# Kernel optimization log

Measured on AMD Instinct MI355X. Metric: run time of the kernel, lower is better.

The kernel has to match this reference:

```python
import jax, jax.numpy as jnp
import numpy as np
import math

H = 16
D_MODEL = 1024
D_K = 64
BS = 8
SEQ = 1024


def setup_inputs() -> dict:
    key = jax.random.key(0)
    ks = jax.random.split(key, 13)
    s = 1.0 / math.sqrt(D_MODEL)
    inp = {
        "q": jax.random.normal(ks[0], (BS, SEQ, D_MODEL), dtype=jnp.float32),
        "k": jax.random.normal(ks[1], (BS, SEQ, D_MODEL), dtype=jnp.float32),
        "v": jax.random.normal(ks[2], (BS, SEQ, D_MODEL), dtype=jnp.float32),
        "mask": jax.random.randint(ks[3], (BS, SEQ, SEQ), 0, 2, dtype=jnp.int32),
        "Wq": jax.random.normal(ks[4], (D_MODEL, D_MODEL), dtype=jnp.float32) * s,
        "bq": jax.random.normal(ks[5], (D_MODEL,), dtype=jnp.float32) * s,
        "Wk": jax.random.normal(ks[6], (D_MODEL, D_MODEL), dtype=jnp.float32) * s,
        "bk": jax.random.normal(ks[7], (D_MODEL,), dtype=jnp.float32) * s,
        "Wv": jax.random.normal(ks[8], (D_MODEL, D_MODEL), dtype=jnp.float32) * s,
        "bv": jax.random.normal(ks[9], (D_MODEL,), dtype=jnp.float32) * s,
        "Wo": jax.random.normal(ks[10], (D_MODEL, D_MODEL), dtype=jnp.float32) * s,
        "bo": jax.random.normal(ks[11], (D_MODEL,), dtype=jnp.float32) * s,
    }
    return inp


def reference(q, k, v, mask, Wq, bq, Wk, bk, Wv, bv, Wo, bo):
    bs, seq, _ = q.shape
    # projections, split heads: [b, h, s, dk]
    def proj(x, W, b):
        y = x @ W + b
        return y.reshape(bs, seq, H, D_K).transpose(0, 2, 1, 3)
    qh = proj(q, Wq, bq)
    kh = proj(k, Wk, bk)
    vh = proj(v, Wv, bv)
    # scaled dot-product attention (dropout is identity in eval mode)
    scores = jnp.einsum("bhqd,bhkd->bhqk", qh, kh) / math.sqrt(D_K)
    scores = jnp.where(mask[:, None, :, :] == 0, jnp.float32(-1e9), scores)
    attn = jax.nn.softmax(scores, axis=-1)
    ctx = jnp.einsum("bhqk,bhkd->bhqd", attn, vh)
    concat = ctx.transpose(0, 2, 1, 3).reshape(bs, seq, D_MODEL)
    return concat @ Wo + bo
```

## Files before the change

### kernel.cpp

```cpp
#include <hip/hip_runtime.h>
#include <hip/hip_bf16.h>

#define HN 16
#define DM 1024
#define DK 64
#define BSZ 8
#define SEQL 1024

typedef __attribute__((ext_vector_type(8))) short bf16x8;
typedef __attribute__((ext_vector_type(4))) short short4v;
typedef __attribute__((ext_vector_type(4))) float f32x4;

__device__ __forceinline__ short f2bf(float f) {
    union { float f; unsigned u; } x; x.f = f;
    unsigned u = x.u + 0x7FFFu + ((x.u >> 16) & 1u);
    return (short)(u >> 16);
}

__device__ __forceinline__ void async16(const void* g, void* ldsbase) {
    __builtin_amdgcn_global_load_lds(
        (const __attribute__((address_space(1))) unsigned int*)g,
        (__attribute__((address_space(3))) unsigned int*)ldsbase, 16, 0, 0);
}

__device__ __forceinline__ short4v pack4bf(float v0, float v1, float v2, float v3) {
    unsigned pk0, pk1;
    asm("v_cvt_pk_bf16_f32 %0, %1, %2" : "=v"(pk0) : "v"(v0), "v"(v1));
    asm("v_cvt_pk_bf16_f32 %0, %1, %2" : "=v"(pk1) : "v"(v2), "v"(v3));
    union { unsigned u[2]; short4v s4; } u_;
    u_.u[0] = pk0; u_.u[1] = pk1;
    return u_.s4;
}

__device__ __forceinline__ bf16x8 pack8bf(f32x4 lo, f32x4 hi) {
    union { short4v h[2]; bf16x8 v; } u_;
    u_.h[0] = pack4bf(lo.x, lo.y, lo.z, lo.w);
    u_.h[1] = pack4bf(hi.x, hi.y, hi.z, hi.w);
    return u_.v;
}

__global__ __launch_bounds__(256) void transpose_cast4(const float* __restrict__ W0,
                                                       const float* __restrict__ W1,
                                                       const float* __restrict__ W2,
                                                       const float* __restrict__ W3,
                                                       short* __restrict__ T0,
                                                       short* __restrict__ T1,
                                                       short* __restrict__ T2,
                                                       short* __restrict__ T3) {
    __shared__ float tile[32][33];
    const int zi = blockIdx.z;
    const float* W = zi == 0 ? W0 : zi == 1 ? W1 : zi == 2 ? W2 : W3;
    short* Wt = zi == 0 ? T0 : zi == 1 ? T1 : zi == 2 ? T2 : T3;
    const int t = threadIdx.x;
    const int k0 = blockIdx.x * 32, n0 = blockIdx.y * 32;
    const int c = t & 31, r = t >> 5;
    #pragma unroll
    for (int p = 0; p < 4; ++p)
        tile[r + 8 * p][c] = W[(size_t)(k0 + r + 8 * p) * DM + n0 + c];
    __syncthreads();
    #pragma unroll
    for (int p = 0; p < 4; ++p)
        Wt[(size_t)(n0 + r + 8 * p) * DM + k0 + c] = f2bf(tile[c][r + 8 * p]);
}

__global__ __launch_bounds__(256) void pack_mask(const int* __restrict__ mask,
                                                 unsigned short* __restrict__ bt) {
    size_t gi = (size_t)blockIdx.x * 256 + threadIdx.x;
    size_t word = gi >> 6;
    int l = threadIdx.x & 63;
    int jperm = ((l >> 2) & 3) * 16 + ((l >> 4) & 3) * 4 + (l & 3);
    size_t row = word >> 4;
    int jblk = (int)(word & 15);
    unsigned long long b = __ballot(mask[row * SEQL + jblk * 64 + jperm] != 0);
    if (l < 4)
        bt[row * 64 + l * 16 + jblk] = (unsigned short)(b >> (l * 16));
}

__global__ __launch_bounds__(256) void gemm_qkv(
    const float* __restrict__ Aq, const float* __restrict__ Ak,
    const float* __restrict__ Av,
    const short* __restrict__ Wqt, const short* __restrict__ Wkt,
    const short* __restrict__ Wvt,
    const float* __restrict__ bqp, const float* __restrict__ bkp,
    const float* __restrict__ bvp,
    short* __restrict__ Cq, short* __restrict__ Ck, short* __restrict__ Cv,
    int zlog) {
    __shared__ __attribute__((aligned(16))) float Af[2][128][32];
    __shared__ __attribute__((aligned(16))) short Bs[2][128][32];
    const int t = threadIdx.x;
    const int lane = t & 63, wv = t >> 6;
    const int wm = (wv >> 1) * 64, wn = (wv & 1) * 64;
    const int quad = lane >> 4, l15 = lane & 15;
    const int tileM = blockIdx.x * 128, tileN = blockIdx.y * 128;
    const int which = blockIdx.z >> zlog;
    const int zz = blockIdx.z & ((1 << zlog) - 1);
    const size_t zoff = (size_t)zz * DM * SEQL;
    const float* A = (which == 0 ? Aq : which == 1 ? Ak : Av) + zoff;
    const short* Wt = which == 0 ? Wqt : which == 1 ? Wkt : Wvt;
    const float* bias = which == 0 ? bqp : which == 1 ? bkp : bvp;
    short* C = (which == 0 ? Cq : which == 1 ? Ck : Cv) + zoff;

    const int arow = t >> 3;
    const int acol = ((t & 7) ^ (arow & 7)) * 4;
    const float* asrc = A + (size_t)(tileM + arow) * DM + acol;
    const int brow = t >> 2;
    const int bcol = (t & 3) * 8;
    const short* bsrc = Wt + (size_t)(tileN + brow) * DM + bcol;

    f32x4 acc[4][4];
    #pragma unroll
    for (int i = 0; i < 4; ++i)
        #pragma unroll
        for (int j = 0; j < 4; ++j) acc[i][j] = {0.f, 0.f, 0.f, 0.f};

    #pragma unroll
    for (int p = 0; p < 4; ++p)
        async16(asrc + (size_t)(p * 32) * DM, &Af[0][p * 32 + wv * 8][0]);
    #pragma unroll
    for (int p = 0; p < 2; ++p)
        async16(bsrc + (size_t)(p * 64) * DM, &Bs[0][p * 64 + wv * 16][0]);
    __syncthreads();

    #pragma unroll 2
    for (int idx = 0; idx < DM / 32; ++idx) {
        const int cur = idx & 1;
        const int k0 = idx * 32;
        if (k0 + 32 < DM) {
            #pragma unroll
            for (int p = 0; p < 4; ++p)
                async16(asrc + (size_t)(p * 32) * DM + (k0 + 32),
                        &Af[cur ^ 1][p * 32 + wv * 8][0]);
            #pragma unroll
            for (int p = 0; p < 2; ++p)
                async16(bsrc + (size_t)(p * 64) * DM + (k0 + 32),
                        &Bs[cur ^ 1][p * 64 + wv * 16][0]);
        }

        bf16x8 a[4], b[4];
        #pragma unroll
        for (int i = 0; i < 4; ++i) {
            const int r = wm + i * 16 + l15;
            const int s = r & 7;
            f32x4 lo = *(const f32x4*)&Af[cur][r][((2 * quad) ^ s) * 4];
            f32x4 hi = *(const f32x4*)&Af[cur][r][((2 * quad + 1) ^ s) * 4];
            a[i] = pack8bf(lo, hi);
        }
        #pragma unroll
        for (int j = 0; j < 4; ++j)
            b[j] = *(const bf16x8*)&Bs[cur][wn + j * 16 + l15][quad * 8];
        #pragma unroll
        for (int i = 0; i < 4; ++i)
            #pragma unroll
            for (int j = 0; j < 4; ++j)
                acc[i][j] = __builtin_amdgcn_mfma_f32_16x16x32_bf16(a[i], b[j], acc[i][j], 0, 0, 0);

        __syncthreads();
    }

    if (which == 2) {
        #pragma unroll
        for (int i = 0; i < 4; ++i)
            #pragma unroll
            for (int j = 0; j < 4; ++j) {
                int rowb = tileM + wm + i * 16 + quad * 4;
                int col = tileN + wn + j * 16 + l15;
                float bb = bias[col];
                short4v s4 = pack4bf(acc[i][j][0] + bb, acc[i][j][1] + bb,
                                     acc[i][j][2] + bb, acc[i][j][3] + bb);
                *(short4v*)(C + (size_t)col * SEQL + rowb) = s4;
            }
    } else {
        #pragma unroll
        for (int i = 0; i < 4; ++i)
            #pragma unroll
            for (int j = 0; j < 4; ++j)
                #pragma unroll
                for (int rr = 0; rr < 4; ++rr) {
                    int row = tileM + wm + i * 16 + quad * 4 + rr;
                    int col = tileN + wn + j * 16 + l15;
                    float v = acc[i][j][rr] + bias[col];
                    C[((size_t)(col >> 6) * SEQL + row) * DK + (col & 63)] = f2bf(v);
                }
    }
}

__global__ __launch_bounds__(256) void gemm_out(const short* __restrict__ A,
                                                const short* __restrict__ Wt,
                                                const float* __restrict__ bias,
                                                float* __restrict__ Cp) {
    __shared__ __attribute__((aligned(16))) short As[2][128][32];
    __shared__ __attribute__((aligned(16))) short Bs[2][128][32];
    const int t = threadIdx.x;
    const int lane = t & 63, wv = t >> 6;
    const int wm = (wv >> 1) * 64, wn = (wv & 1) * 64;
    const int quad = lane >> 4, l15 = lane & 15;
    const int tileM = blockIdx.x * 128, tileN = blockIdx.y * 128;
    const size_t zoff = (size_t)blockIdx.z * DM * SEQL;
    const short* Az = A + zoff;

    const int sr = wv * 16 + (lane >> 2);
    const int sc = (lane & 3) * 8;
    const short* asrc = Az + (size_t)(tileM + sr) * DM + sc;
    const short* bsrc = Wt + (size_t)(tileN + sr) * DM + sc;

    f32x4 acc[4][4];
    #pragma unroll
    for (int i = 0; i < 4; ++i)
        #pragma unroll
        for (int j = 0; j < 4; ++j) acc[i][j] = {0.f, 0.f, 0.f, 0.f};

    #pragma unroll
    for (int p = 0; p < 2; ++p) {
        async16(asrc + (size_t)p * 64 * DM, &As[0][p * 64 + wv * 16][0]);
        async16(bsrc + (size_t)p * 64 * DM, &Bs[0][p * 64 + wv * 16][0]);
    }
    __syncthreads();

    #pragma unroll 2
    for (int idx = 0; idx < DM / 32; ++idx) {
        const int cur = idx & 1;
        const int k0 = idx * 32;
        if (k0 + 32 < DM) {
            #pragma unroll
            for (int p = 0; p < 2; ++p) {
                async16(asrc + (size_t)p * 64 * DM + (k0 + 32),
                        &As[cur ^ 1][p * 64 + wv * 16][0]);
                async16(bsrc + (size_t)p * 64 * DM + (k0 + 32),
                        &Bs[cur ^ 1][p * 64 + wv * 16][0]);
            }
        }

        bf16x8 a[4], b[4];
        #pragma unroll
        for (int i = 0; i < 4; ++i) a[i] = *(const bf16x8*)&As[cur][wm + i * 16 + l15][quad * 8];
        #pragma unroll
        for (int j = 0; j < 4; ++j) b[j] = *(const bf16x8*)&Bs[cur][wn + j * 16 + l15][quad * 8];
        #pragma unroll
        for (int i = 0; i < 4; ++i)
            #pragma unroll
            for (int j = 0; j < 4; ++j)
                acc[i][j] = __builtin_amdgcn_mfma_f32_16x16x32_bf16(a[i], b[j], acc[i][j], 0, 0, 0);

        __syncthreads();
    }

    float* C = Cp + zoff;
    #pragma unroll
    for (int i = 0; i < 4; ++i)
        #pragma unroll
        for (int j = 0; j < 4; ++j)
            #pragma unroll
            for (int rr = 0; rr < 4; ++rr) {
                int row = tileM + wm + i * 16 + quad * 4 + rr;
                int col = tileN + wn + j * 16 + l15;
                C[(size_t)row * DM + col] = acc[i][j][rr] + bias[col];
            }
}

template <bool USE_BITS>
__global__ __launch_bounds__(256) void attn_mfma(const short* __restrict__ Qw,
                                                 const short* __restrict__ Kw,
                                                 const short* __restrict__ Vt,
                                                 const void* __restrict__ maskp,
                                                 short* __restrict__ ctx) {
    __shared__ __attribute__((aligned(16))) short Kbuf[2][64 * 64];
    __shared__ __attribute__((aligned(16))) short Vbuf[2][64 * 64];
    __shared__ __attribute__((aligned(16))) short Ps[4][16 * 64];
    const int t = threadIdx.x;
    const int lane = t & 63, w = t >> 6;
    const int quad = lane >> 4, l15 = lane & 15;
    const int nwg = gridDim.x;
    const int cpx = nwg >> 3;
    const int vb = (blockIdx.x & 7) * cpx + (blockIdx.x >> 3);
    const int q0 = (vb & 15) * 64;
    const int h = (vb >> 4) & 15;
    const int z = vb >> 8;
    const size_t zoff = (size_t)z * DM * SEQL;
    const short* Qb = Qw + zoff + (size_t)h * SEQL * DK;
    const short* Kb = Kw + zoff + (size_t)h * SEQL * DK;
    const short* Vb = Vt + zoff + (size_t)h * DK * SEQL;
    const int qrow = q0 + w * 16 + l15;
    const int x = (l15 & 7) << 3;

    bf16x8 qf0 = *(const bf16x8*)(Qb + (size_t)qrow * DK + quad * 8);
    bf16x8 qf1 = *(const bf16x8*)(Qb + (size_t)qrow * DK + 32 + quad * 8);

    unsigned long long mA = 0, mB = 0, mC = 0, mD = 0;
    if (USE_BITS) {
        const unsigned long long* bt64 = (const unsigned long long*)
            ((const unsigned short*)maskp + (size_t)z * SEQL * 64 +
             (size_t)qrow * 64 + quad * 16);
        mA = bt64[0]; mB = bt64[1]; mC = bt64[2]; mD = bt64[3];
    }

    const int r0 = t >> 3;
    const int kc = ((t & 7) ^ (r0 & 7)) * 8;
    const short* ks0 = Kb + (size_t)r0 * DK + kc;
    const short* ks1 = ks0 + 32 * DK;
    const short* vs0 = Vb + (size_t)r0 * SEQL + kc;
    const short* vs1 = vs0 + 32 * SEQL;

    async16(ks0, &Kbuf[0][w * 512]);
    async16(ks1, &Kbuf[0][2048 + w * 512]);
    async16(vs0, &Vbuf[0][w * 512]);
    async16(vs1, &Vbuf[0][2048 + w * 512]);
    ks0 += 64 * DK; ks1 += 64 * DK; vs0 += 64; vs1 += 64;
    __syncthreads();

    f32x4 o[4];
    #pragma unroll
    for (int td = 0; td < 4; ++td) o[td] = {0.f, 0.f, 0.f, 0.f};
    float Lacc = 0.f;

    #pragma unroll 2
    for (int iter = 0; iter < 16; ++iter) {
        const int cur = iter & 1;
        if (iter < 15) {
            async16(ks0, &Kbuf[cur ^ 1][w * 512]);
            async16(ks1, &Kbuf[cur ^ 1][2048 + w * 512]);
            async16(vs0, &Vbuf[cur ^ 1][w * 512]);
            async16(vs1, &Vbuf[cur ^ 1][2048 + w * 512]);
            ks0 += 64 * DK; ks1 += 64 * DK; vs0 += 64; vs1 += 64;
        }

        const short* Kl = &Kbuf[cur][0];
        const short* Vl = &Vbuf[cur][0];
        unsigned mw16 = 0;
        if (USE_BITS) {
            unsigned long long t01 = (iter & 4) ? mB : mA;
            unsigned long long t23 = (iter & 4) ? mD : mC;
            unsigned long long tw = (iter & 8) ? t23 : t01;
            mw16 = (unsigned)(tw >> ((iter & 3) * 16)) & 0xFFFFu;
        }

        #pragma unroll
        for (int tn = 0; tn < 4; ++tn) {
            const int r = tn * 16 + l15;
            bf16x8 ak0 = *(const bf16x8*)&Kl[r * 64 + ((quad * 8) ^ x)];
            bf16x8 ak1 = *(const bf16x8*)&Kl[r * 64 + ((32 + quad * 8) ^ x)];
            f32x4 s = {0.f, 0.f, 0.f, 0.f};
            __builtin_amdgcn_s_setprio(1);
            s = __builtin_amdgcn_mfma_f32_16x16x32_bf16(ak0, qf0, s, 0, 0, 0);
            s = __builtin_amdgcn_mfma_f32_16x16x32_bf16(ak1, qf1, s, 0, 0, 0);
            __builtin_amdgcn_s_setprio(0);
            float pv[4];
            const unsigned nib = USE_BITS ? (mw16 >> (tn * 4)) & 0xFu : 0u;
            #pragma unroll
            for (int rr = 0; rr < 4; ++rr) {
                bool keep;
                if (USE_BITS) {
                    keep = (nib >> rr) & 1u;
                } else {
                    const int* mi = (const int*)maskp + (size_t)z * SEQL * SEQL;
                    keep = mi[(size_t)qrow * SEQL + iter * 64 + tn * 16 + quad * 4 + rr] != 0;
                }
                float e = __expf(s[rr] * 0.125f);
                pv[rr] = keep ? e : 0.0f;
                Lacc += pv[rr];
            }
            *(short4v*)&Ps[w][l15 * 64 + ((tn * 16 + quad * 4) ^ x)] =
                pack4bf(pv[0], pv[1], pv[2], pv[3]);
        }
        bf16x8 ap0 = *(const bf16x8*)&Ps[w][l15 * 64 + ((quad * 8) ^ x)];
        bf16x8 ap1 = *(const bf16x8*)&Ps[w][l15 * 64 + ((32 + quad * 8) ^ x)];
        __builtin_amdgcn_s_setprio(1);
        #pragma unroll
        for (int td = 0; td < 4; ++td) {
            const int r = td * 16 + l15;
            bf16x8 bv0 = *(const bf16x8*)&Vl[r * 64 + ((quad * 8) ^ x)];
            bf16x8 bv1 = *(const bf16x8*)&Vl[r * 64 + ((32 + quad * 8) ^ x)];
            o[td] = __builtin_amdgcn_mfma_f32_16x16x32_bf16(ap0, bv0, o[td], 0, 0, 0);
            o[td] = __builtin_amdgcn_mfma_f32_16x16x32_bf16(ap1, bv1, o[td], 0, 0, 0);
        }
        __builtin_amdgcn_s_setprio(0);

        __syncthreads();
    }

    Lacc += __shfl_xor(Lacc, 16);
    Lacc += __shfl_xor(Lacc, 32);
    float Linv = 1.0f / Lacc;
    float Linv4[4];
    #pragma unroll
    for (int rr = 0; rr < 4; ++rr)
        Linv4[rr] = __shfl(Linv, quad * 4 + rr);

    short* cb = ctx + zoff;
    #pragma unroll
    for (int td = 0; td < 4; ++td)
        #pragma unroll
        for (int rr = 0; rr < 4; ++rr) {
            int rq = q0 + w * 16 + quad * 4 + rr;
            int cd = h * 64 + td * 16 + l15;
            cb[(size_t)rq * DM + cd] = f2bf(o[td][rr] * Linv4[rr]);
        }
}

extern "C" void kernel_launch(void* const* d_in, const int* in_sizes, int n_in,
                              void* d_out, int out_size, void* d_ws, size_t ws_size,
                              hipStream_t stream) {
    const float* q  = (const float*)d_in[0];
    const float* k  = (const float*)d_in[1];
    const float* v  = (const float*)d_in[2];
    const int* mask = (const int*)d_in[3];
    const float* Wq = (const float*)d_in[4];
    const float* bq = (const float*)d_in[5];
    const float* Wk = (const float*)d_in[6];
    const float* bk = (const float*)d_in[7];
    const float* Wv = (const float*)d_in[8];
    const float* bv = (const float*)d_in[9];
    const float* Wo = (const float*)d_in[10];
    const float* bo = (const float*)d_in[11];
    float* out = (float*)d_out;

    const size_t MB = (size_t)1 << 20;
    const size_t MEL = (size_t)1024 * 1024;
    char* base = (char*)d_ws;

    short* Wqt = (short*)(base + 0 * 2 * MB);
    short* Wkt = (short*)(base + 1 * 2 * MB);
    short* Wvt = (short*)(base + 2 * 2 * MB);
    short* Wot = (short*)(base + 3 * 2 * MB);

    int zdim;
    bool use_bits;
    if      (ws_size >= 74 * MB) { zdim = 8; use_bits = true; }
    else if (ws_size >= 42 * MB) { zdim = 4; use_bits = true; }
    else if (ws_size >= 26 * MB) { zdim = 2; use_bits = true; }
    else if (ws_size >= 18 * MB) { zdim = 1; use_bits = true; }
    else                         { zdim = 1; use_bits = false; }
    const int zlog = (zdim == 8) ? 3 : (zdim == 4) ? 2 : (zdim == 2) ? 1 : 0;

    unsigned short* bits = (unsigned short*)(base + 8 * MB);
    char* bufs = base + (use_bits ? 9 : 8) * MB;
    const size_t bufB = (size_t)zdim * 2 * MB;
    short* Qw  = (short*)(bufs);
    short* Kw  = (short*)(bufs + bufB);
    short* Vw  = (short*)(bufs + 2 * bufB);
    short* ctx = (short*)(bufs + 3 * bufB);

    transpose_cast4<<<dim3(32, 32, 4), 256, 0, stream>>>(Wq, Wk, Wv, Wo,
                                                         Wqt, Wkt, Wvt, Wot);
    if (use_bits)
        pack_mask<<<(BSZ * SEQL * SEQL) / 256, 256, 0, stream>>>(mask, bits);

    const int iters = BSZ / zdim;
    for (int it = 0; it < iters; ++it) {
        const size_t boff = (size_t)it * zdim * MEL;
        const float* qb = q + boff;
        const float* kb = k + boff;
        const float* vb = v + boff;
        float* ob = out + boff;
        const void* mb = use_bits
            ? (const void*)(bits + (size_t)it * zdim * SEQL * 64)
            : (const void*)(mask + (size_t)it * zdim * SEQL * SEQL);

        gemm_qkv<<<dim3(8, 8, 3 * zdim), 256, 0, stream>>>(
            qb, kb, vb, Wqt, Wkt, Wvt, bq, bk, bv, Qw, Kw, Vw, zlog);

        const int attnBlocks = 16 * 16 * zdim;
        if (use_bits)
            attn_mfma<true><<<attnBlocks, 256, 0, stream>>>(Qw, Kw, Vw, mb, ctx);
        else
            attn_mfma<false><<<attnBlocks, 256, 0, stream>>>(Qw, Kw, Vw, mb, ctx);

        gemm_out<<<dim3(8, 8, zdim), 256, 0, stream>>>(ctx, Wot, bo, ob);
    }
}
```

Before: 395.5 us.

## Convert QKV activation tiles to bf16 before LDS store; drop setprio in attention

The QKV projection GEMM used to copy fp32 activation tiles into LDS asynchronously and convert them to bf16 on every fragment read. It now loads fp32 into registers, packs to bf16 once, and writes a padded bf16 tile (row stride 40). This halves LDS footprint and per-fragment LDS read traffic, and each element is converted only once instead of once per warp that reads it. The cost is register prefetching through VGPRs in place of direct-to-LDS loads, which adds register pressure and needs the global load latency hidden behind the MFMAs. Separately, the s_setprio hints around the MFMAs in the attention kernel are removed.

```diff
diff --git a/kernel.cpp b/kernel.cpp
--- a/kernel.cpp
+++ b/kernel.cpp
@@ -85,7 +85,7 @@
     const float* __restrict__ bvp,
     short* __restrict__ Cq, short* __restrict__ Ck, short* __restrict__ Cv,
     int zlog) {
-    __shared__ __attribute__((aligned(16))) float Af[2][128][32];
+    __shared__ __attribute__((aligned(16))) short As[2][128][40];
     __shared__ __attribute__((aligned(16))) short Bs[2][128][32];
     const int t = threadIdx.x;
     const int lane = t & 63, wv = t >> 6;
@@ -100,8 +100,8 @@
     const float* bias = which == 0 ? bqp : which == 1 ? bkp : bvp;
     short* C = (which == 0 ? Cq : which == 1 ? Ck : Cv) + zoff;
 
-    const int arow = t >> 3;
-    const int acol = ((t & 7) ^ (arow & 7)) * 4;
+    const int arow = t >> 1;
+    const int acol = (t & 1) * 16;
     const float* asrc = A + (size_t)(tileM + arow) * DM + acol;
     const int brow = t >> 2;
     const int bcol = (t & 3) * 8;
@@ -113,23 +113,30 @@
         #pragma unroll
         for (int j = 0; j < 4; ++j) acc[i][j] = {0.f, 0.f, 0.f, 0.f};
 
-    #pragma unroll
-    for (int p = 0; p < 4; ++p)
-        async16(asrc + (size_t)(p * 32) * DM, &Af[0][p * 32 + wv * 8][0]);
-    #pragma unroll
-    for (int p = 0; p < 2; ++p)
-        async16(bsrc + (size_t)(p * 64) * DM, &Bs[0][p * 64 + wv * 16][0]);
+    {
+        f32x4 r0 = *(const f32x4*)(asrc + 0);
+        f32x4 r1 = *(const f32x4*)(asrc + 4);
+        f32x4 r2 = *(const f32x4*)(asrc + 8);
+        f32x4 r3 = *(const f32x4*)(asrc + 12);
+        #pragma unroll
+        for (int p = 0; p < 2; ++p)
+            async16(bsrc + (size_t)(p * 64) * DM, &Bs[0][p * 64 + wv * 16][0]);
+        *(bf16x8*)&As[0][arow][acol] = pack8bf(r0, r1);
+        *(bf16x8*)&As[0][arow][acol + 8] = pack8bf(r2, r3);
+    }
     __syncthreads();
 
     #pragma unroll 2
     for (int idx = 0; idx < DM / 32; ++idx) {
         const int cur = idx & 1;
         const int k0 = idx * 32;
-        if (k0 + 32 < DM) {
-            #pragma unroll
-            for (int p = 0; p < 4; ++p)
-                async16(asrc + (size_t)(p * 32) * DM + (k0 + 32),
-                        &Af[cur ^ 1][p * 32 + wv * 8][0]);
+        const bool more = (k0 + 32 < DM);
+        f32x4 n0, n1, n2, n3;
+        if (more) {
+            n0 = *(const f32x4*)(asrc + k0 + 32);
+            n1 = *(const f32x4*)(asrc + k0 + 36);
+            n2 = *(const f32x4*)(asrc + k0 + 40);
+            n3 = *(const f32x4*)(asrc + k0 + 44);
             #pragma unroll
             for (int p = 0; p < 2; ++p)
                 async16(bsrc + (size_t)(p * 64) * DM + (k0 + 32),
@@ -138,13 +145,8 @@
 
         bf16x8 a[4], b[4];
         #pragma unroll
-        for (int i = 0; i < 4; ++i) {
-            const int r = wm + i * 16 + l15;
-            const int s = r & 7;
-            f32x4 lo = *(const f32x4*)&Af[cur][r][((2 * quad) ^ s) * 4];
-            f32x4 hi = *(const f32x4*)&Af[cur][r][((2 * quad + 1) ^ s) * 4];
-            a[i] = pack8bf(lo, hi);
-        }
+        for (int i = 0; i < 4; ++i)
+            a[i] = *(const bf16x8*)&As[cur][wm + i * 16 + l15][quad * 8];
         #pragma unroll
         for (int j = 0; j < 4; ++j)
             b[j] = *(const bf16x8*)&Bs[cur][wn + j * 16 + l15][quad * 8];
@@ -154,6 +156,10 @@
             for (int j = 0; j < 4; ++j)
                 acc[i][j] = __builtin_amdgcn_mfma_f32_16x16x32_bf16(a[i], b[j], acc[i][j], 0, 0, 0);
 
+        if (more) {
+            *(bf16x8*)&As[cur ^ 1][arow][acol] = pack8bf(n0, n1);
+            *(bf16x8*)&As[cur ^ 1][arow][acol + 8] = pack8bf(n2, n3);
+        }
         __syncthreads();
     }
 
@@ -339,10 +345,8 @@
             bf16x8 ak0 = *(const bf16x8*)&Kl[r * 64 + ((quad * 8) ^ x)];
             bf16x8 ak1 = *(const bf16x8*)&Kl[r * 64 + ((32 + quad * 8) ^ x)];
             f32x4 s = {0.f, 0.f, 0.f, 0.f};
-            __builtin_amdgcn_s_setprio(1);
             s = __builtin_amdgcn_mfma_f32_16x16x32_bf16(ak0, qf0, s, 0, 0, 0);
             s = __builtin_amdgcn_mfma_f32_16x16x32_bf16(ak1, qf1, s, 0, 0, 0);
-            __builtin_amdgcn_s_setprio(0);
             float pv[4];
             const unsigned nib = USE_BITS ? (mw16 >> (tn * 4)) & 0xFu : 0u;
             #pragma unroll
@@ -363,7 +367,6 @@
         }
         bf16x8 ap0 = *(const bf16x8*)&Ps[w][l15 * 64 + ((quad * 8) ^ x)];
         bf16x8 ap1 = *(const bf16x8*)&Ps[w][l15 * 64 + ((32 + quad * 8) ^ x)];
-        __builtin_amdgcn_s_setprio(1);
         #pragma unroll
         for (int td = 0; td < 4; ++td) {
             const int r = td * 16 + l15;
@@ -372,7 +375,6 @@
             o[td] = __builtin_amdgcn_mfma_f32_16x16x32_bf16(ap0, bv0, o[td], 0, 0, 0);
             o[td] = __builtin_amdgcn_mfma_f32_16x16x32_bf16(ap1, bv1, o[td], 0, 0, 0);
         }
-        __builtin_amdgcn_s_setprio(0);
 
         __syncthreads();
     }
```

New measurement: 414.6 us. +4.8%, slower.
